# Kernel tuning notes

Measured on AMD Instinct MI355X. Metric: run time of the kernel, lower is better.

The kernel has to match this reference:

```python
import jax, jax.numpy as jnp
import numpy as np

IN_FEATURES = 512
NUM_CENTERS = 2048
BATCH = 16384


def setup_inputs() -> dict:
    key = jax.random.key(0)
    kx, kc = jax.random.split(key)
    x = jax.random.normal(kx, (BATCH, IN_FEATURES), dtype=jnp.float32)
    centers = jax.random.normal(kc, (NUM_CENTERS, IN_FEATURES), dtype=jnp.float32)
    beta = jnp.ones((NUM_CENTERS,), dtype=jnp.float32)
    return {"x": x, "centers": centers, "beta": beta}


def reference(x, centers, beta):
    x_sq = jnp.sum(x * x, axis=-1, keepdims=True)            # (B, 1)
    c_sq = jnp.sum(centers * centers, axis=-1)                # (M,)
    cross = jnp.einsum('bd,md->bm', x, centers)               # (B, M)
    dist_sq = x_sq + c_sq[None, :] - 2.0 * cross              # (B, M)
    return jnp.exp(-beta[None, :] * dist_sq)
```

## Files before the change

### kernel.cpp

```cpp
#include <hip/hip_runtime.h>
#include <stdint.h>

#define IN_F   512
#define N_CTR  2048
#define BATCH  16384

#define BM 128
#define BN 128
#define BK 64
#define NKT (IN_F / BK)

using bf16x8  = __attribute__((ext_vector_type(8))) short;
using f32x4   = __attribute__((ext_vector_type(4))) float;
using ushort8 = __attribute__((ext_vector_type(8))) unsigned short;

typedef const __attribute__((address_space(1))) void* gptr_t;
typedef __attribute__((address_space(3))) void* lptr_t;

static __device__ __forceinline__ unsigned short f2bf(float f) {
    uint32_t u = __builtin_bit_cast(uint32_t, f);
    uint32_t r = u + 0x7fffu + ((u >> 16) & 1u);
    return (unsigned short)(r >> 16);
}

__global__ void convert_all(const float* __restrict__ x,
                            const float* __restrict__ c,
                            unsigned short* __restrict__ xb,
                            unsigned short* __restrict__ cb,
                            float* __restrict__ xsq,
                            float* __restrict__ csq) {
    const int wave = threadIdx.x >> 6;
    const int lane = threadIdx.x & 63;
    const int row  = blockIdx.x * 4 + wave;

    const float* src;
    unsigned short* dst;
    float* sq;
    int r;
    if (row < BATCH) { src = x; dst = xb; sq = xsq; r = row; }
    else             { src = c; dst = cb; sq = csq; r = row - BATCH; }

    const float* rp = src + (size_t)r * IN_F + lane * 8;
    float4 a = *reinterpret_cast<const float4*>(rp);
    float4 b = *reinterpret_cast<const float4*>(rp + 4);
    float ss = a.x*a.x + a.y*a.y + a.z*a.z + a.w*a.w
             + b.x*b.x + b.y*b.y + b.z*b.z + b.w*b.w;
    ushort8 o;
    o[0]=f2bf(a.x); o[1]=f2bf(a.y); o[2]=f2bf(a.z); o[3]=f2bf(a.w);
    o[4]=f2bf(b.x); o[5]=f2bf(b.y); o[6]=f2bf(b.z); o[7]=f2bf(b.w);
    *reinterpret_cast<ushort8*>(dst + (size_t)r * IN_F + lane * 8) = o;
    #pragma unroll
    for (int off = 32; off > 0; off >>= 1) ss += __shfl_down(ss, off);
    if (lane == 0) sq[r] = ss;
}

__launch_bounds__(256, 2)
__global__ void rbf_gemm(const unsigned short* __restrict__ xb,
                         const unsigned short* __restrict__ cb,
                         const float* __restrict__ xsq,
                         const float* __restrict__ csq,
                         const float* __restrict__ beta,
                         float* __restrict__ out) {
    __shared__ unsigned short As[2][BM * BK];
    __shared__ unsigned short Bs[2][BN * BK];

    const int tid  = threadIdx.x;
    const int wid  = tid >> 6;
    const int lane = tid & 63;
    const int wr   = wid >> 1;
    const int wc   = wid & 1;

    const int ntn = N_CTR / BN;
    const int tm  = blockIdx.x / ntn;
    const int tn  = blockIdx.x % ntn;

    const int srow = (wid * 4) * 8 + (lane >> 3);
    const int scol = (lane & 7) * 8;
    const unsigned short* gA0 = xb + (size_t)(tm * BM + srow) * IN_F + scol;
    const unsigned short* gB0 = cb + (size_t)(tn * BN + srow) * IN_F + scol;

    f32x4 acc[4][4] = {};

    auto stage = [&](int buf, int kt) {
        const int kbase = kt * BK;
        #pragma unroll
        for (int i = 0; i < 4; ++i) {
            const unsigned short* ga = gA0 + (size_t)(i * 8) * IN_F + kbase;
            const unsigned short* gb = gB0 + (size_t)(i * 8) * IN_F + kbase;
            __builtin_amdgcn_global_load_lds((gptr_t)ga, (lptr_t)(&As[buf][(wid * 4 + i) * 512]), 16, 0, 0);
            __builtin_amdgcn_global_load_lds((gptr_t)gb, (lptr_t)(&Bs[buf][(wid * 4 + i) * 512]), 16, 0, 0);
        }
    };

    auto compute = [&](int buf) {
        #pragma unroll
        for (int kk = 0; kk < 2; ++kk) {
            bf16x8 af[4], bfr[4];
            const int kreg = kk * 32 + (lane >> 4) * 8;
            #pragma unroll
            for (int mi = 0; mi < 4; ++mi)
                af[mi] = *reinterpret_cast<const bf16x8*>(
                    &As[buf][(wr * 64 + mi * 16 + (lane & 15)) * BK + kreg]);
            #pragma unroll
            for (int ni = 0; ni < 4; ++ni)
                bfr[ni] = *reinterpret_cast<const bf16x8*>(
                    &Bs[buf][(wc * 64 + ni * 16 + (lane & 15)) * BK + kreg]);
            #pragma unroll
            for (int mi = 0; mi < 4; ++mi)
                #pragma unroll
                for (int ni = 0; ni < 4; ++ni)
                    acc[mi][ni] = __builtin_amdgcn_mfma_f32_16x16x32_bf16(
                        af[mi], bfr[ni], acc[mi][ni], 0, 0, 0);
        }
    };

    stage(0, 0);
    __syncthreads();

    int cur = 0;
    #pragma unroll
    for (int kt = 0; kt < NKT - 1; ++kt) {
        stage(cur ^ 1, kt + 1);
        compute(cur);
        __syncthreads();
        cur ^= 1;
    }
    compute(cur);

    const int row0 = tm * BM + wr * 64;
    const int col0 = tn * BN + wc * 64;
    #pragma unroll
    for (int ni = 0; ni < 4; ++ni) {
        const int col = col0 + ni * 16 + (lane & 15);
        const float bt = beta[col];
        const float cs = csq[col];
        #pragma unroll
        for (int mi = 0; mi < 4; ++mi) {
            #pragma unroll
            for (int j = 0; j < 4; ++j) {
                const int row = row0 + mi * 16 + (lane >> 4) * 4 + j;
                const float d = xsq[row] + cs - 2.0f * acc[mi][ni][j];
                out[(size_t)row * N_CTR + col] = __expf(-bt * d);
            }
        }
    }
}

__global__ void rbf_naive(const float* __restrict__ x,
                          const float* __restrict__ c,
                          const float* __restrict__ beta,
                          float* __restrict__ out) {
    __shared__ float xs[IN_F];
    const int row = blockIdx.x;
    const int col = blockIdx.y * 128 + threadIdx.x;
    for (int i = threadIdx.x; i < IN_F; i += 128)
        xs[i] = x[(size_t)row * IN_F + i];
    __syncthreads();
    const float* cp = c + (size_t)col * IN_F;
    float d = 0.f;
    #pragma unroll 4
    for (int k = 0; k < IN_F; k += 4) {
        float4 cv = *reinterpret_cast<const float4*>(cp + k);
        float t0 = xs[k + 0] - cv.x;
        float t1 = xs[k + 1] - cv.y;
        float t2 = xs[k + 2] - cv.z;
        float t3 = xs[k + 3] - cv.w;
        d += t0 * t0 + t1 * t1 + t2 * t2 + t3 * t3;
    }
    out[(size_t)row * N_CTR + col] = __expf(-beta[col] * d);
}

extern "C" void kernel_launch(void* const* d_in, const int* in_sizes, int n_in,
                              void* d_out, int out_size, void* d_ws, size_t ws_size,
                              hipStream_t stream) {
    const float* x    = (const float*)d_in[0];
    const float* c    = (const float*)d_in[1];
    const float* beta = (const float*)d_in[2];
    float* out        = (float*)d_out;

    const size_t need = (size_t)BATCH * IN_F * 2 + (size_t)N_CTR * IN_F * 2
                      + (size_t)BATCH * 4 + (size_t)N_CTR * 4;
    if (ws_size >= need) {
        unsigned short* xbuf = (unsigned short*)d_ws;
        unsigned short* cbuf = xbuf + (size_t)BATCH * IN_F;
        float* xsq = (float*)(cbuf + (size_t)N_CTR * IN_F);
        float* csq = xsq + BATCH;
        convert_all<<<(BATCH + N_CTR) / 4, 256, 0, stream>>>(x, c, xbuf, cbuf, xsq, csq);
        rbf_gemm<<<(BATCH / BM) * (N_CTR / BN), 256, 0, stream>>>(
            xbuf, cbuf, xsq, csq, beta, out);
    } else {
        rbf_naive<<<dim3(BATCH, N_CTR / 128), 128, 0, stream>>>(x, c, beta, out);
    }
}
```

Measured before the change: 75.37 us.

## Single-buffer LDS for higher occupancy and swizzle block-to-tile mapping

Replaces the double-buffered LDS pipeline with a single buffer and two barriers per k-step, halving shared memory so three workgroups can fit per CU (launch bounds raised to 3). It also remaps block IDs with a stride-8 swizzle so that concurrently scheduled blocks touch different tile rows and columns, aiming at better cache or XCD locality. The trade-off is that global-to-LDS loads no longer overlap with MFMA compute within a block, so latency hiding now depends on the other resident workgroups.

```diff
diff --git a/kernel.cpp b/kernel.cpp
--- a/kernel.cpp
+++ b/kernel.cpp
@@ -54,15 +54,15 @@
     if (lane == 0) sq[r] = ss;
 }
 
-__launch_bounds__(256, 2)
+__launch_bounds__(256, 3)
 __global__ void rbf_gemm(const unsigned short* __restrict__ xb,
                          const unsigned short* __restrict__ cb,
                          const float* __restrict__ xsq,
                          const float* __restrict__ csq,
                          const float* __restrict__ beta,
                          float* __restrict__ out) {
-    __shared__ unsigned short As[2][BM * BK];
-    __shared__ unsigned short Bs[2][BN * BK];
+    __shared__ unsigned short As[BM * BK];
+    __shared__ unsigned short Bs[BN * BK];
 
     const int tid  = threadIdx.x;
     const int wid  = tid >> 6;
@@ -70,9 +70,13 @@
     const int wr   = wid >> 1;
     const int wc   = wid & 1;
 
+    const int nwg = gridDim.x;
+    const int bid = blockIdx.x;
+    const int swz = (bid & 7) * (nwg >> 3) + (bid >> 3);
+
     const int ntn = N_CTR / BN;
-    const int tm  = blockIdx.x / ntn;
-    const int tn  = blockIdx.x % ntn;
+    const int tm  = swz / ntn;
+    const int tn  = swz % ntn;
 
     const int srow = (wid * 4) * 8 + (lane >> 3);
     const int scol = (lane & 7) * 8;
@@ -81,18 +85,17 @@
 
     f32x4 acc[4][4] = {};
 
-    auto stage = [&](int buf, int kt) {
+    for (int kt = 0; kt < NKT; ++kt) {
         const int kbase = kt * BK;
         #pragma unroll
         for (int i = 0; i < 4; ++i) {
             const unsigned short* ga = gA0 + (size_t)(i * 8) * IN_F + kbase;
             const unsigned short* gb = gB0 + (size_t)(i * 8) * IN_F + kbase;
-            __builtin_amdgcn_global_load_lds((gptr_t)ga, (lptr_t)(&As[buf][(wid * 4 + i) * 512]), 16, 0, 0);
-            __builtin_amdgcn_global_load_lds((gptr_t)gb, (lptr_t)(&Bs[buf][(wid * 4 + i) * 512]), 16, 0, 0);
+            __builtin_amdgcn_global_load_lds((gptr_t)ga, (lptr_t)(As + (wid * 4 + i) * 512), 16, 0, 0);
+            __builtin_amdgcn_global_load_lds((gptr_t)gb, (lptr_t)(Bs + (wid * 4 + i) * 512), 16, 0, 0);
         }
-    };
+        __syncthreads();
 
-    auto compute = [&](int buf) {
         #pragma unroll
         for (int kk = 0; kk < 2; ++kk) {
             bf16x8 af[4], bfr[4];
@@ -100,11 +103,11 @@
             #pragma unroll
             for (int mi = 0; mi < 4; ++mi)
                 af[mi] = *reinterpret_cast<const bf16x8*>(
-                    &As[buf][(wr * 64 + mi * 16 + (lane & 15)) * BK + kreg]);
+                    &As[(wr * 64 + mi * 16 + (lane & 15)) * BK + kreg]);
             #pragma unroll
             for (int ni = 0; ni < 4; ++ni)
                 bfr[ni] = *reinterpret_cast<const bf16x8*>(
-                    &Bs[buf][(wc * 64 + ni * 16 + (lane & 15)) * BK + kreg]);
+                    &Bs[(wc * 64 + ni * 16 + (lane & 15)) * BK + kreg]);
             #pragma unroll
             for (int mi = 0; mi < 4; ++mi)
                 #pragma unroll
@@ -112,20 +115,8 @@
                     acc[mi][ni] = __builtin_amdgcn_mfma_f32_16x16x32_bf16(
                         af[mi], bfr[ni], acc[mi][ni], 0, 0, 0);
         }
-    };
-
-    stage(0, 0);
-    __syncthreads();
-
-    int cur = 0;
-    #pragma unroll
-    for (int kt = 0; kt < NKT - 1; ++kt) {
-        stage(cur ^ 1, kt + 1);
-        compute(cur);
         __syncthreads();
-        cur ^= 1;
     }
-    compute(cur);
 
     const int row0 = tm * BM + wr * 64;
     const int col0 = tn * BN + wc * 64;
```

Measured after the change: 73.54 us. 1.02x faster.
